# Optimization experiments

Hardware: AMD Instinct MI355X
Metric: run time of the kernel (lower is better)

Reference implementation:

```python
import jax, jax.numpy as jnp
import numpy as np

B, S, H, F, E, K = 2, 1024, 2048, 5504, 8, 2


def setup_inputs() -> dict:
    key = jax.random.key(0)
    k0, k1, k2, k3, k4 = jax.random.split(key, 5)
    x = jax.random.normal(k0, (B, S, H), dtype=jnp.float32)
    # nn.Linear weight layout is [out, in]
    router_w = jax.random.normal(k1, (E, H), dtype=jnp.float32) * 0.02   # router gate
    gate_w = jax.random.normal(k2, (E, F, H), dtype=jnp.float32) * 0.02  # per-expert gate_proj
    up_w = jax.random.normal(k3, (E, F, H), dtype=jnp.float32) * 0.02    # per-expert up_proj
    down_w = jax.random.normal(k4, (E, H, F), dtype=jnp.float32) * 0.02  # per-expert down_proj
    return {"x": x, "router_w": router_w, "gate_w": gate_w, "up_w": up_w, "down_w": down_w}


def reference(x, router_w, gate_w, up_w, down_w):
    b, s, h = x.shape
    xf = x.reshape(-1, h)                                   # [T, H]
    # --- router: top-k over expert logits, softmax over the k selected ---
    logits = xf @ router_w.T                                # [T, E]
    top_v, top_i = jax.lax.top_k(logits, K)                 # [T, K]
    probs = jax.nn.softmax(top_v.astype(jnp.float32), axis=-1).astype(logits.dtype)
    # per-token combine weight for each expert (0 if not selected)
    combine = jnp.sum(jax.nn.one_hot(top_i, E, dtype=x.dtype) * probs[..., None], axis=1)  # [T, E]
    # --- experts: SwiGLU, batched over the expert axis ---
    g = jnp.einsum('th,efh->etf', xf, gate_w)               # [E, T, F]
    u = jnp.einsum('th,efh->etf', xf, up_w)                 # [E, T, F]
    y = jnp.einsum('etf,ehf->eth', jax.nn.silu(g) * u, down_w)  # [E, T, H]
    # --- combine: weighted sum over experts ---
    out = jnp.einsum('te,eth->th', combine, y)              # [T, H]
    return out.reshape(b, s, h)
```

## Files before the change

kernel.cpp:

```cpp
#include <hip/hip_runtime.h>
#include <cstdint>
#include <cstddef>

#define H 2048
#define F 5504
#define E 8
#define T 2048
#define ROWCAP 5120

typedef __bf16 bf16x8 __attribute__((ext_vector_type(8)));
typedef float f32x4 __attribute__((ext_vector_type(4)));

#define AS1(p) ((const __attribute__((address_space(1))) void*)(p))
#define AS3(p) ((__attribute__((address_space(3))) void*)(p))

__global__ void router_kernel(const float* __restrict__ x,
                              const float* __restrict__ rw,
                              int* __restrict__ cnt,
                              int* __restrict__ list_t,
                              float* __restrict__ list_w) {
    const int wv = threadIdx.x >> 6;
    const int lane = threadIdx.x & 63;
    const int t = blockIdx.x * 4 + wv;
    const float4* xp = (const float4*)(x + (size_t)t * H) + lane * 8;
    float4 xv[8];
#pragma unroll
    for (int i = 0; i < 8; ++i) xv[i] = xp[i];
    float lg[E];
#pragma unroll
    for (int e = 0; e < E; ++e) {
        const float4* wp = (const float4*)(rw + (size_t)e * H) + lane * 8;
        float acc = 0.f;
#pragma unroll
        for (int i = 0; i < 8; ++i) {
            float4 w4 = wp[i];
            acc += xv[i].x * w4.x + xv[i].y * w4.y + xv[i].z * w4.z + xv[i].w * w4.w;
        }
#pragma unroll
        for (int o = 32; o > 0; o >>= 1) acc += __shfl_xor(acc, o, 64);
        lg[e] = acc;
    }
    if (lane == 0) {
        float v0 = -3e38f, v1 = -3e38f;
        int i0 = 0, i1 = 0;
#pragma unroll
        for (int e = 0; e < E; ++e) {
            float v = lg[e];
            if (v > v0) { v1 = v0; i1 = i0; v0 = v; i0 = e; }
            else if (v > v1) { v1 = v; i1 = e; }
        }
        float p0 = 1.f / (1.f + __expf(v1 - v0));
        float p1 = 1.f - p0;
        int s0 = atomicAdd(&cnt[i0], 1);
        list_t[i0 * T + s0] = t;
        list_w[i0 * T + s0] = p0;
        int s1 = atomicAdd(&cnt[i1], 1);
        list_t[i1 * T + s1] = t;
        list_w[i1 * T + s1] = p1;
    }
}

__global__ void offsets_kernel(const int* __restrict__ cnt, int* __restrict__ off) {
    if (threadIdx.x == 0) {
        int acc = 0;
        for (int e = 0; e < E; ++e) {
            off[e] = acc;
            acc += (cnt[e] + 127) & ~127;
        }
    }
}

__global__ void gather_kernel(const float* __restrict__ x,
                              const int* __restrict__ cnt,
                              const int* __restrict__ off,
                              const int* __restrict__ list_t,
                              const float* __restrict__ list_w,
                              __bf16* __restrict__ Abuf,
                              int* __restrict__ row_t,
                              float* __restrict__ row_w) {
    const int e = blockIdx.y, slot = blockIdx.x;
    if (slot >= cnt[e]) return;
    const int row = off[e] + slot;
    if (threadIdx.x == 0) {
        row_t[row] = list_t[e * T + slot];
        row_w[row] = list_w[e * T + slot];
    }
    const int t = list_t[e * T + slot];
    const float4* src = (const float4*)(x + (size_t)t * H);
    float4 a = src[threadIdx.x * 2], b = src[threadIdx.x * 2 + 1];
    bf16x8 o;
    o[0] = (__bf16)a.x; o[1] = (__bf16)a.y; o[2] = (__bf16)a.z; o[3] = (__bf16)a.w;
    o[4] = (__bf16)b.x; o[5] = (__bf16)b.y; o[6] = (__bf16)b.z; o[7] = (__bf16)b.w;
    *(bf16x8*)(Abuf + (size_t)row * H + threadIdx.x * 8) = o;
}

__global__ void __launch_bounds__(256, 2)
gateup_kernel(const __bf16* __restrict__ Abuf,
              const float* __restrict__ gw,
              const float* __restrict__ uw,
              const int* __restrict__ cnt,
              const int* __restrict__ off,
              const float* __restrict__ row_w,
              __bf16* __restrict__ act) {
    const int e = blockIdx.z;
    const int count = cnt[e];
    const int mt = blockIdx.y;
    if (mt * 128 >= count) return;
    const int n0 = blockIdx.x * 128;
    const int rowbase = off[e] + mt * 128;

    __shared__ __bf16 As[128 * 32];
    __shared__ __bf16 Gs[128 * 32];
    __shared__ __bf16 Us[128 * 32];

    const int tid = threadIdx.x;
    const int wv = tid >> 6, lane = tid & 63;
    const int wr = wv >> 1, wc = wv & 1;
    const int quad = lane >> 4, l16 = lane & 15;

    f32x4 accG[4][4] = {};
    f32x4 accU[4][4] = {};

    const __bf16* abase = Abuf + (size_t)rowbase * H;
    const float* gbase = gw + (size_t)e * F * H + (size_t)n0 * H;
    const float* ubase = uw + (size_t)e * F * H + (size_t)n0 * H;

    const int arow = lane >> 2;
    const int acol = (lane & 3) * 8;
    const int wrow = tid >> 1;
    const int kh = (tid & 1) * 16;

    for (int k0 = 0; k0 < H; k0 += 32) {
#pragma unroll
        for (int i = 0; i < 2; ++i) {
            const int seg = wv * 2 + i;
            const __bf16* gp = abase + (size_t)(seg * 16 + arow) * H + k0 + acol;
            __builtin_amdgcn_global_load_lds(AS1(gp), AS3(As + seg * 512), 16, 0, 0);
        }
        {
            const float4* gp = (const float4*)(gbase + (size_t)wrow * H + k0 + kh);
            float4 f0 = gp[0], f1 = gp[1], f2 = gp[2], f3 = gp[3];
            bf16x8 h0, h1;
            h0[0] = (__bf16)f0.x; h0[1] = (__bf16)f0.y; h0[2] = (__bf16)f0.z; h0[3] = (__bf16)f0.w;
            h0[4] = (__bf16)f1.x; h0[5] = (__bf16)f1.y; h0[6] = (__bf16)f1.z; h0[7] = (__bf16)f1.w;
            h1[0] = (__bf16)f2.x; h1[1] = (__bf16)f2.y; h1[2] = (__bf16)f2.z; h1[3] = (__bf16)f2.w;
            h1[4] = (__bf16)f3.x; h1[5] = (__bf16)f3.y; h1[6] = (__bf16)f3.z; h1[7] = (__bf16)f3.w;
            *(bf16x8*)(Gs + wrow * 32 + kh) = h0;
            *(bf16x8*)(Gs + wrow * 32 + kh + 8) = h1;
            const float4* up = (const float4*)(ubase + (size_t)wrow * H + k0 + kh);
            f0 = up[0]; f1 = up[1]; f2 = up[2]; f3 = up[3];
            h0[0] = (__bf16)f0.x; h0[1] = (__bf16)f0.y; h0[2] = (__bf16)f0.z; h0[3] = (__bf16)f0.w;
            h0[4] = (__bf16)f1.x; h0[5] = (__bf16)f1.y; h0[6] = (__bf16)f1.z; h0[7] = (__bf16)f1.w;
            h1[0] = (__bf16)f2.x; h1[1] = (__bf16)f2.y; h1[2] = (__bf16)f2.z; h1[3] = (__bf16)f2.w;
            h1[4] = (__bf16)f3.x; h1[5] = (__bf16)f3.y; h1[6] = (__bf16)f3.z; h1[7] = (__bf16)f3.w;
            *(bf16x8*)(Us + wrow * 32 + kh) = h0;
            *(bf16x8*)(Us + wrow * 32 + kh + 8) = h1;
        }
        __syncthreads();

        bf16x8 af[4], gf[4], uf[4];
#pragma unroll
        for (int i = 0; i < 4; ++i)
            af[i] = *(const bf16x8*)(As + (wr * 64 + i * 16 + l16) * 32 + quad * 8);
#pragma unroll
        for (int j = 0; j < 4; ++j) {
            gf[j] = *(const bf16x8*)(Gs + (wc * 64 + j * 16 + l16) * 32 + quad * 8);
            uf[j] = *(const bf16x8*)(Us + (wc * 64 + j * 16 + l16) * 32 + quad * 8);
        }
#pragma unroll
        for (int i = 0; i < 4; ++i)
#pragma unroll
            for (int j = 0; j < 4; ++j) {
                accG[i][j] = __builtin_amdgcn_mfma_f32_16x16x32_bf16(af[i], gf[j], accG[i][j], 0, 0, 0);
                accU[i][j] = __builtin_amdgcn_mfma_f32_16x16x32_bf16(af[i], uf[j], accU[i][j], 0, 0, 0);
            }
        __syncthreads();
    }

#pragma unroll
    for (int i = 0; i < 4; ++i) {
        const int ml = wr * 64 + i * 16 + quad * 4;
#pragma unroll
        for (int r = 0; r < 4; ++r) {
            const float w = row_w[rowbase + ml + r];
            __bf16* arow_p = act + (size_t)(rowbase + ml + r) * F + n0;
#pragma unroll
            for (int j = 0; j < 4; ++j) {
                const int nl = wc * 64 + j * 16 + l16;
                float g = accG[i][j][r], u = accU[i][j][r];
                float s = g / (1.f + __expf(-g));
                arow_p[nl] = (__bf16)(s * u * w);
            }
        }
    }
}

__global__ void __launch_bounds__(256, 2)
down_kernel(const __bf16* __restrict__ act,
            const float* __restrict__ dw,
            const int* __restrict__ cnt,
            const int* __restrict__ off,
            const int* __restrict__ row_t,
            float* __restrict__ out) {
    const int e = blockIdx.z;
    const int count = cnt[e];
    const int mt = blockIdx.y;
    if (mt * 128 >= count) return;
    const int h0 = blockIdx.x * 128;
    const int rowbase = off[e] + mt * 128;

    __shared__ __bf16 As[128 * 32];
    __shared__ __bf16 Ws[128 * 32];

    const int tid = threadIdx.x;
    const int wv = tid >> 6, lane = tid & 63;
    const int wr = wv >> 1, wc = wv & 1;
    const int quad = lane >> 4, l16 = lane & 15;

    f32x4 acc[4][4] = {};

    const __bf16* abase = act + (size_t)rowbase * F;
    const float* wbase = dw + (size_t)e * H * F + (size_t)h0 * F;

    const int arow = lane >> 2;
    const int acol = (lane & 3) * 8;
    const int wrow = tid >> 1;
    const int kh = (tid & 1) * 16;

    for (int k0 = 0; k0 < F; k0 += 32) {
#pragma unroll
        for (int i = 0; i < 2; ++i) {
            const int seg = wv * 2 + i;
            const __bf16* gp = abase + (size_t)(seg * 16 + arow) * F + k0 + acol;
            __builtin_amdgcn_global_load_lds(AS1(gp), AS3(As + seg * 512), 16, 0, 0);
        }
        {
            const float4* gp = (const float4*)(wbase + (size_t)wrow * F + k0 + kh);
            float4 f0 = gp[0], f1 = gp[1], f2 = gp[2], f3 = gp[3];
            bf16x8 h0v, h1v;
            h0v[0] = (__bf16)f0.x; h0v[1] = (__bf16)f0.y; h0v[2] = (__bf16)f0.z; h0v[3] = (__bf16)f0.w;
            h0v[4] = (__bf16)f1.x; h0v[5] = (__bf16)f1.y; h0v[6] = (__bf16)f1.z; h0v[7] = (__bf16)f1.w;
            h1v[0] = (__bf16)f2.x; h1v[1] = (__bf16)f2.y; h1v[2] = (__bf16)f2.z; h1v[3] = (__bf16)f2.w;
            h1v[4] = (__bf16)f3.x; h1v[5] = (__bf16)f3.y; h1v[6] = (__bf16)f3.z; h1v[7] = (__bf16)f3.w;
            *(bf16x8*)(Ws + wrow * 32 + kh) = h0v;
            *(bf16x8*)(Ws + wrow * 32 + kh + 8) = h1v;
        }
        __syncthreads();

        bf16x8 af[4], bf[4];
#pragma unroll
        for (int i = 0; i < 4; ++i)
            af[i] = *(const bf16x8*)(As + (wr * 64 + i * 16 + l16) * 32 + quad * 8);
#pragma unroll
        for (int j = 0; j < 4; ++j)
            bf[j] = *(const bf16x8*)(Ws + (wc * 64 + j * 16 + l16) * 32 + quad * 8);
#pragma unroll
        for (int i = 0; i < 4; ++i)
#pragma unroll
            for (int j = 0; j < 4; ++j)
                acc[i][j] = __builtin_amdgcn_mfma_f32_16x16x32_bf16(af[i], bf[j], acc[i][j], 0, 0, 0);
        __syncthreads();
    }

#pragma unroll
    for (int i = 0; i < 4; ++i) {
        const int ml = wr * 64 + i * 16 + quad * 4;
#pragma unroll
        for (int r = 0; r < 4; ++r) {
            const int lr = mt * 128 + ml + r;
            if (lr < count) {
                const int t = row_t[rowbase + ml + r];
                float* orow = out + (size_t)t * H + h0;
#pragma unroll
                for (int j = 0; j < 4; ++j)
                    atomicAdd(&orow[wc * 64 + j * 16 + l16], acc[i][j][r]);
            }
        }
    }
}

extern "C" void kernel_launch(void* const* d_in, const int* in_sizes, int n_in,
                              void* d_out, int out_size, void* d_ws, size_t ws_size,
                              hipStream_t stream) {
    const float* x  = (const float*)d_in[0];
    const float* rw = (const float*)d_in[1];
    const float* gw = (const float*)d_in[2];
    const float* uw = (const float*)d_in[3];
    const float* dw = (const float*)d_in[4];
    float* out = (float*)d_out;
    char* ws = (char*)d_ws;

    int*   cnt    = (int*)(ws + 0);
    int*   off    = (int*)(ws + 256);
    int*   list_t = (int*)(ws + 1024);
    float* list_w = (float*)(ws + 1024 + 65536);
    int*   row_t  = (int*)(ws + 1024 + 2 * 65536);
    float* row_w  = (float*)(ws + 1024 + 2 * 65536 + 20480);
    __bf16* Abuf  = (__bf16*)(ws + 262144);
    __bf16* act   = (__bf16*)(ws + 262144 + (size_t)ROWCAP * H * 2);

    hipMemsetAsync(d_out, 0, (size_t)out_size * sizeof(float), stream);
    hipMemsetAsync(ws, 0, 1024, stream);

    router_kernel<<<T / 4, 256, 0, stream>>>(x, rw, cnt, list_t, list_w);
    offsets_kernel<<<1, 64, 0, stream>>>(cnt, off);
    gather_kernel<<<dim3(T, E), 256, 0, stream>>>(x, cnt, off, list_t, list_w, Abuf, row_t, row_w);
    gateup_kernel<<<dim3(F / 128, T / 128, E), 256, 0, stream>>>(Abuf, gw, uw, cnt, off, row_w, act);
    down_kernel<<<dim3(H / 128, T / 128, E), 256, 0, stream>>>(act, dw, cnt, off, row_t, out);
}
```

Measured before the change: 1.656 ms.

## Double-buffer LDS tiles and enlarge M tile to 256 rows in expert GEMMs

Both expert GEMM kernels now use a 256x128 tile with 512 threads and double-buffered shared memory. The next K-slice of activations and weights is prefetched (weights via registers) while MFMAs run on the current buffer, leaving one barrier per iteration. The grid is reordered so the M tile is the fast index, which may improve weight reuse in L2, and expert padding and workspace capacity grow to 256-row multiples. The bigger tile halves how often each weight slice is re-read across M tiles, but it raises register and LDS pressure and adds padded work for experts with fewer tokens.

```diff
diff --git a/kernel.cpp b/kernel.cpp
--- a/kernel.cpp
+++ b/kernel.cpp
@@ -6,7 +6,11 @@
 #define F 5504
 #define E 8
 #define T 2048
-#define ROWCAP 5120
+#define ROWCAP 6144
+
+#define BM 256
+#define BN 128
+#define BK 32
 
 typedef __bf16 bf16x8 __attribute__((ext_vector_type(8)));
 typedef float f32x4 __attribute__((ext_vector_type(4)));
@@ -65,7 +69,7 @@
         int acc = 0;
         for (int e = 0; e < E; ++e) {
             off[e] = acc;
-            acc += (cnt[e] + 127) & ~127;
+            acc += (cnt[e] + 255) & ~255;
         }
     }
 }
@@ -94,7 +98,7 @@
     *(bf16x8*)(Abuf + (size_t)row * H + threadIdx.x * 8) = o;
 }
 
-__global__ void __launch_bounds__(256, 2)
+__global__ void __launch_bounds__(512, 2)
 gateup_kernel(const __bf16* __restrict__ Abuf,
               const float* __restrict__ gw,
               const float* __restrict__ uw,
@@ -104,14 +108,14 @@
               __bf16* __restrict__ act) {
     const int e = blockIdx.z;
     const int count = cnt[e];
-    const int mt = blockIdx.y;
-    if (mt * 128 >= count) return;
-    const int n0 = blockIdx.x * 128;
-    const int rowbase = off[e] + mt * 128;
-
-    __shared__ __bf16 As[128 * 32];
-    __shared__ __bf16 Gs[128 * 32];
-    __shared__ __bf16 Us[128 * 32];
+    const int mt = blockIdx.x;
+    if (mt * BM >= count) return;
+    const int n0 = blockIdx.y * BN;
+    const int rowbase = off[e] + mt * BM;
+
+    __shared__ __bf16 As[2][BM * BK];
+    __shared__ __bf16 Gs[2][BN * BK];
+    __shared__ __bf16 Us[2][BN * BK];
 
     const int tid = threadIdx.x;
     const int wv = tid >> 6, lane = tid & 63;
@@ -127,55 +131,81 @@
 
     const int arow = lane >> 2;
     const int acol = (lane & 3) * 8;
-    const int wrow = tid >> 1;
-    const int kh = (tid & 1) * 16;
-
-    for (int k0 = 0; k0 < H; k0 += 32) {
-#pragma unroll
-        for (int i = 0; i < 2; ++i) {
-            const int seg = wv * 2 + i;
-            const __bf16* gp = abase + (size_t)(seg * 16 + arow) * H + k0 + acol;
-            __builtin_amdgcn_global_load_lds(AS1(gp), AS3(As + seg * 512), 16, 0, 0);
-        }
-        {
-            const float4* gp = (const float4*)(gbase + (size_t)wrow * H + k0 + kh);
-            float4 f0 = gp[0], f1 = gp[1], f2 = gp[2], f3 = gp[3];
-            bf16x8 h0, h1;
-            h0[0] = (__bf16)f0.x; h0[1] = (__bf16)f0.y; h0[2] = (__bf16)f0.z; h0[3] = (__bf16)f0.w;
-            h0[4] = (__bf16)f1.x; h0[5] = (__bf16)f1.y; h0[6] = (__bf16)f1.z; h0[7] = (__bf16)f1.w;
-            h1[0] = (__bf16)f2.x; h1[1] = (__bf16)f2.y; h1[2] = (__bf16)f2.z; h1[3] = (__bf16)f2.w;
-            h1[4] = (__bf16)f3.x; h1[5] = (__bf16)f3.y; h1[6] = (__bf16)f3.z; h1[7] = (__bf16)f3.w;
-            *(bf16x8*)(Gs + wrow * 32 + kh) = h0;
-            *(bf16x8*)(Gs + wrow * 32 + kh + 8) = h1;
-            const float4* up = (const float4*)(ubase + (size_t)wrow * H + k0 + kh);
-            f0 = up[0]; f1 = up[1]; f2 = up[2]; f3 = up[3];
-            h0[0] = (__bf16)f0.x; h0[1] = (__bf16)f0.y; h0[2] = (__bf16)f0.z; h0[3] = (__bf16)f0.w;
-            h0[4] = (__bf16)f1.x; h0[5] = (__bf16)f1.y; h0[6] = (__bf16)f1.z; h0[7] = (__bf16)f1.w;
-            h1[0] = (__bf16)f2.x; h1[1] = (__bf16)f2.y; h1[2] = (__bf16)f2.z; h1[3] = (__bf16)f2.w;
-            h1[4] = (__bf16)f3.x; h1[5] = (__bf16)f3.y; h1[6] = (__bf16)f3.z; h1[7] = (__bf16)f3.w;
-            *(bf16x8*)(Us + wrow * 32 + kh) = h0;
-            *(bf16x8*)(Us + wrow * 32 + kh + 8) = h1;
-        }
+    const int wrow = tid >> 2;
+    const int wk = (tid & 3) * 8;
+
+    float4 pg0, pg1, pu0, pu1;
+
+#define STAGE_A(buf, k0)                                                                     \
+    do {                                                                                     \
+        _Pragma("unroll")                                                                    \
+        for (int i_ = 0; i_ < 2; ++i_) {                                                     \
+            const int seg_ = i_ * 8 + wv;                                                    \
+            const __bf16* gp_ = abase + (size_t)(seg_ * 16 + arow) * H + (k0) + acol;        \
+            __builtin_amdgcn_global_load_lds(AS1(gp_), AS3(&As[buf][seg_ * 512]), 16, 0, 0); \
+        }                                                                                    \
+    } while (0)
+
+#define LOAD_W(k0)                                                                   \
+    do {                                                                             \
+        const float4* gp_ = (const float4*)(gbase + (size_t)wrow * H + (k0) + wk);   \
+        pg0 = gp_[0]; pg1 = gp_[1];                                                  \
+        const float4* up_ = (const float4*)(ubase + (size_t)wrow * H + (k0) + wk);   \
+        pu0 = up_[0]; pu1 = up_[1];                                                  \
+    } while (0)
+
+#define WRITE_W(buf)                                                                             \
+    do {                                                                                         \
+        bf16x8 hg_, hu_;                                                                         \
+        hg_[0] = (__bf16)pg0.x; hg_[1] = (__bf16)pg0.y; hg_[2] = (__bf16)pg0.z; hg_[3] = (__bf16)pg0.w; \
+        hg_[4] = (__bf16)pg1.x; hg_[5] = (__bf16)pg1.y; hg_[6] = (__bf16)pg1.z; hg_[7] = (__bf16)pg1.w; \
+        hu_[0] = (__bf16)pu0.x; hu_[1] = (__bf16)pu0.y; hu_[2] = (__bf16)pu0.z; hu_[3] = (__bf16)pu0.w; \
+        hu_[4] = (__bf16)pu1.x; hu_[5] = (__bf16)pu1.y; hu_[6] = (__bf16)pu1.z; hu_[7] = (__bf16)pu1.w; \
+        *(bf16x8*)(&Gs[buf][wrow * BK + wk]) = hg_;                                              \
+        *(bf16x8*)(&Us[buf][wrow * BK + wk]) = hu_;                                              \
+    } while (0)
+
+#define COMPUTE(buf)                                                                             \
+    do {                                                                                         \
+        bf16x8 af_[4], gf_[4], uf_[4];                                                           \
+        _Pragma("unroll")                                                                        \
+        for (int i_ = 0; i_ < 4; ++i_)                                                           \
+            af_[i_] = *(const bf16x8*)(&As[buf][(wr * 64 + i_ * 16 + l16) * BK + quad * 8]);     \
+        _Pragma("unroll")                                                                        \
+        for (int j_ = 0; j_ < 4; ++j_) {                                                         \
+            gf_[j_] = *(const bf16x8*)(&Gs[buf][(wc * 64 + j_ * 16 + l16) * BK + quad * 8]);     \
+            uf_[j_] = *(const bf16x8*)(&Us[buf][(wc * 64 + j_ * 16 + l16) * BK + quad * 8]);     \
+        }                                                                                        \
+        _Pragma("unroll")                                                                        \
+        for (int i_ = 0; i_ < 4; ++i_)                                                           \
+            _Pragma("unroll")                                                                    \
+            for (int j_ = 0; j_ < 4; ++j_) {                                                     \
+                accG[i_][j_] = __builtin_amdgcn_mfma_f32_16x16x32_bf16(af_[i_], gf_[j_], accG[i_][j_], 0, 0, 0); \
+                accU[i_][j_] = __builtin_amdgcn_mfma_f32_16x16x32_bf16(af_[i_], uf_[j_], accU[i_][j_], 0, 0, 0); \
+            }                                                                                    \
+    } while (0)
+
+    STAGE_A(0, 0);
+    LOAD_W(0);
+    WRITE_W(0);
+    __syncthreads();
+
+    const int NT = H / BK;
+    for (int t = 0; t < NT - 1; ++t) {
+        const int cur = t & 1, nxt = cur ^ 1;
+        const int k1 = (t + 1) * BK;
+        STAGE_A(nxt, k1);
+        LOAD_W(k1);
+        COMPUTE(cur);
+        WRITE_W(nxt);
         __syncthreads();
-
-        bf16x8 af[4], gf[4], uf[4];
-#pragma unroll
-        for (int i = 0; i < 4; ++i)
-            af[i] = *(const bf16x8*)(As + (wr * 64 + i * 16 + l16) * 32 + quad * 8);
-#pragma unroll
-        for (int j = 0; j < 4; ++j) {
-            gf[j] = *(const bf16x8*)(Gs + (wc * 64 + j * 16 + l16) * 32 + quad * 8);
-            uf[j] = *(const bf16x8*)(Us + (wc * 64 + j * 16 + l16) * 32 + quad * 8);
-        }
-#pragma unroll
-        for (int i = 0; i < 4; ++i)
-#pragma unroll
-            for (int j = 0; j < 4; ++j) {
-                accG[i][j] = __builtin_amdgcn_mfma_f32_16x16x32_bf16(af[i], gf[j], accG[i][j], 0, 0, 0);
-                accU[i][j] = __builtin_amdgcn_mfma_f32_16x16x32_bf16(af[i], uf[j], accU[i][j], 0, 0, 0);
-            }
-        __syncthreads();
-    }
+    }
+    COMPUTE((NT - 1) & 1);
+
+#undef STAGE_A
+#undef LOAD_W
+#undef WRITE_W
+#undef COMPUTE
 
 #pragma unroll
     for (int i = 0; i < 4; ++i) {
@@ -195,7 +225,7 @@
     }
 }
 
-__global__ void __launch_bounds__(256, 2)
+__global__ void __launch_bounds__(512, 2)
 down_kernel(const __bf16* __restrict__ act,
             const float* __restrict__ dw,
             const int* __restrict__ cnt,
@@ -204,13 +234,13 @@
             float* __restrict__ out) {
     const int e = blockIdx.z;
     const int count = cnt[e];
-    const int mt = blockIdx.y;
-    if (mt * 128 >= count) return;
-    const int h0 = blockIdx.x * 128;
-    const int rowbase = off[e] + mt * 128;
-
-    __shared__ __bf16 As[128 * 32];
-    __shared__ __bf16 Ws[128 * 32];
+    const int mt = blockIdx.x;
+    if (mt * BM >= count) return;
+    const int h0 = blockIdx.y * BN;
+    const int rowbase = off[e] + mt * BM;
+
+    __shared__ __bf16 As[2][BM * BK];
+    __shared__ __bf16 Ws[2][BN * BK];
 
     const int tid = threadIdx.x;
     const int wv = tid >> 6, lane = tid & 63;
@@ -224,50 +254,79 @@
 
     const int arow = lane >> 2;
     const int acol = (lane & 3) * 8;
-    const int wrow = tid >> 1;
-    const int kh = (tid & 1) * 16;
-
-    for (int k0 = 0; k0 < F; k0 += 32) {
-#pragma unroll
-        for (int i = 0; i < 2; ++i) {
-            const int seg = wv * 2 + i;
-            const __bf16* gp = abase + (size_t)(seg * 16 + arow) * F + k0 + acol;
-            __builtin_amdgcn_global_load_lds(AS1(gp), AS3(As + seg * 512), 16, 0, 0);
-        }
-        {
-            const float4* gp = (const float4*)(wbase + (size_t)wrow * F + k0 + kh);
-            float4 f0 = gp[0], f1 = gp[1], f2 = gp[2], f3 = gp[3];
-            bf16x8 h0v, h1v;
-            h0v[0] = (__bf16)f0.x; h0v[1] = (__bf16)f0.y; h0v[2] = (__bf16)f0.z; h0v[3] = (__bf16)f0.w;
-            h0v[4] = (__bf16)f1.x; h0v[5] = (__bf16)f1.y; h0v[6] = (__bf16)f1.z; h0v[7] = (__bf16)f1.w;
-            h1v[0] = (__bf16)f2.x; h1v[1] = (__bf16)f2.y; h1v[2] = (__bf16)f2.z; h1v[3] = (__bf16)f2.w;
-            h1v[4] = (__bf16)f3.x; h1v[5] = (__bf16)f3.y; h1v[6] = (__bf16)f3.z; h1v[7] = (__bf16)f3.w;
-            *(bf16x8*)(Ws + wrow * 32 + kh) = h0v;
-            *(bf16x8*)(Ws + wrow * 32 + kh + 8) = h1v;
-        }
+    const int wrow = tid >> 2;
+    const int wk = (tid & 3) * 8;
+
+    float4 pw0, pw1;
+
+#define STAGE_A(buf, k0)                                                                     \
+    do {                                                                                     \
+        _Pragma("unroll")                                                                    \
+        for (int i_ = 0; i_ < 2; ++i_) {                                                     \
+            const int seg_ = i_ * 8 + wv;                                                    \
+            const __bf16* gp_ = abase + (size_t)(seg_ * 16 + arow) * F + (k0) + acol;        \
+            __builtin_amdgcn_global_load_lds(AS1(gp_), AS3(&As[buf][seg_ * 512]), 16, 0, 0); \
+        }                                                                                    \
+    } while (0)
+
+#define LOAD_W(k0)                                                                   \
+    do {                                                                             \
+        const float4* gp_ = (const float4*)(wbase + (size_t)wrow * F + (k0) + wk);   \
+        pw0 = gp_[0]; pw1 = gp_[1];                                                  \
+    } while (0)
+
+#define WRITE_W(buf)                                                                             \
+    do {                                                                                         \
+        bf16x8 hw_;                                                                              \
+        hw_[0] = (__bf16)pw0.x; hw_[1] = (__bf16)pw0.y; hw_[2] = (__bf16)pw0.z; hw_[3] = (__bf16)pw0.w; \
+        hw_[4] = (__bf16)pw1.x; hw_[5] = (__bf16)pw1.y; hw_[6] = (__bf16)pw1.z; hw_[7] = (__bf16)pw1.w; \
+        *(bf16x8*)(&Ws[buf][wrow * BK + wk]) = hw_;                                              \
+    } while (0)
+
+#define COMPUTE(buf)                                                                             \
+    do {                                                                                         \
+        bf16x8 af_[4], bf_[4];                                                                   \
+        _Pragma("unroll")                                                                        \
+        for (int i_ = 0; i_ < 4; ++i_)                                                           \
+            af_[i_] = *(const bf16x8*)(&As[buf][(wr * 64 + i_ * 16 + l16) * BK + quad * 8]);     \
+        _Pragma("unroll")                                                                        \
+        for (int j_ = 0; j_ < 4; ++j_)                                                           \
+            bf_[j_] = *(const bf16x8*)(&Ws[buf][(wc * 64 + j_ * 16 + l16) * BK + quad * 8]);     \
+        _Pragma("unroll")                                                                        \
+        for (int i_ = 0; i_ < 4; ++i_)                                                           \
+            _Pragma("unroll")                                                                    \
+            for (int j_ = 0; j_ < 4; ++j_)                                                       \
+                acc[i_][j_] = __builtin_amdgcn_mfma_f32_16x16x32_bf16(af_[i_], bf_[j_], acc[i_][j_], 0, 0, 0); \
+    } while (0)
+
+    STAGE_A(0, 0);
+    LOAD_W(0);
+    WRITE_W(0);
+    __syncthreads();
+
+    const int NT = F / BK;
+    for (int t = 0; t < NT - 1; ++t) {
+        const int cur = t & 1, nxt = cur ^ 1;
+        const int k1 = (t + 1) * BK;
+        STAGE_A(nxt, k1);
+        LOAD_W(k1);
+        COMPUTE(cur);
+        WRITE_W(nxt);
         __syncthreads();
-
-        bf16x8 af[4], bf[4];
-#pragma unroll
-        for (int i = 0; i < 4; ++i)
-            af[i] = *(const bf16x8*)(As + (wr * 64 + i * 16 + l16) * 32 + quad * 8);
-#pragma unroll
-        for (int j = 0; j < 4; ++j)
-            bf[j] = *(const bf16x8*)(Ws + (wc * 64 + j * 16 + l16) * 32 + quad * 8);
-#pragma unroll
-        for (int i = 0; i < 4; ++i)
-#pragma unroll
-            for (int j = 0; j < 4; ++j)
-                acc[i][j] = __builtin_amdgcn_mfma_f32_16x16x32_bf16(af[i], bf[j], acc[i][j], 0, 0, 0);
-        __syncthreads();
-    }
+    }
+    COMPUTE((NT - 1) & 1);
+
+#undef STAGE_A
+#undef LOAD_W
+#undef WRITE_W
+#undef COMPUTE
 
 #pragma unroll
     for (int i = 0; i < 4; ++i) {
         const int ml = wr * 64 + i * 16 + quad * 4;
 #pragma unroll
         for (int r = 0; r < 4; ++r) {
-            const int lr = mt * 128 + ml + r;
+            const int lr = mt * BM + ml + r;
             if (lr < count) {
                 const int t = row_t[rowbase + ml + r];
                 float* orow = out + (size_t)t * H + h0;
@@ -295,7 +354,7 @@
     int*   list_t = (int*)(ws + 1024);
     float* list_w = (float*)(ws + 1024 + 65536);
     int*   row_t  = (int*)(ws + 1024 + 2 * 65536);
-    float* row_w  = (float*)(ws + 1024 + 2 * 65536 + 20480);
+    float* row_w  = (float*)(ws + 1024 + 2 * 65536 + ROWCAP * 4);
     __bf16* Abuf  = (__bf16*)(ws + 262144);
     __bf16* act   = (__bf16*)(ws + 262144 + (size_t)ROWCAP * H * 2);
 
@@ -305,6 +364,6 @@
     router_kernel<<<T / 4, 256, 0, stream>>>(x, rw, cnt, list_t, list_w);
     offsets_kernel<<<1, 64, 0, stream>>>(cnt, off);
     gather_kernel<<<dim3(T, E), 256, 0, stream>>>(x, cnt, off, list_t, list_w, Abuf, row_t, row_w);
-    gateup_kernel<<<dim3(F / 128, T / 128, E), 256, 0, stream>>>(Abuf, gw, uw, cnt, off, row_w, act);
-    down_kernel<<<dim3(H / 128, T / 128, E), 256, 0, stream>>>(act, dw, cnt, off, row_t, out);
-}
+    gateup_kernel<<<dim3(8, F / BN, E), 512, 0, stream>>>(Abuf, gw, uw, cnt, off, row_w, act);
+    down_kernel<<<dim3(8, H / BN, E), 512, 0, stream>>>(act, dw, cnt, off, row_t, out);
+}
```

New measurement: 2.702 ms. 63.2% more time.
